# Performance work log

Hardware: AMD Instinct MI355X
Metric: run time of the kernel (lower is better)

Reference implementation:

```python
import jax, jax.numpy as jnp
import numpy as np


def setup_inputs() -> dict:
    key = jax.random.key(0)
    k1, k2 = jax.random.split(key)
    B, S_LOGITS, S_PEN, V = 4, 512, 128, 32000
    logits = jax.random.normal(k1, (B, S_LOGITS, V), dtype=jnp.float32)
    penalty_sequence = jax.random.randint(k2, (B, S_PEN), 0, V, dtype=jnp.int64)
    return {"logits": logits, "penalty_sequence": penalty_sequence, "pad_id": 0}


def reference(logits, penalty_sequence, pad_id):
    B, _, V = logits.shape
    # presence mask over vocab per batch: scatter-max of (id != pad) indicator.
    # Equivalent to onehot(...).sum(-2).clip(max=1) without the (B,S,V) blowup.
    valid = (penalty_sequence != pad_id).astype(logits.dtype)  # (B, S_pen)
    mask = jnp.zeros((B, V), dtype=logits.dtype)
    mask = mask.at[jnp.arange(B)[:, None], penalty_sequence].max(valid)  # (B, V)
    probs = jax.nn.softmax(logits, axis=-1)  # (B, S, V)
    # loss = (mask[:, None, :] * probs).sum(-1)
    return jnp.einsum('bsv,bv->bs', probs, mask)
```

## Files before the change

kernel.cpp:

```cpp
#include <hip/hip_runtime.h>
#include <hip/hip_bf16.h>


#define SPEN 128
#define NWORDS 1000
#define BLOCK 256

__global__ __launch_bounds__(BLOCK) void suppression_loss_kernel(
    const float* __restrict__ logits,
    const int* __restrict__ seq,
    const int* __restrict__ pad_ptr,
    float* __restrict__ out,
    int S, int V) {

    __shared__ unsigned int maskw[NWORDS];
    __shared__ float sd[BLOCK / 64], sn[BLOCK / 64];

    const int row = blockIdx.x;
    const int b   = row / S;
    const int t   = threadIdx.x;
    const int pad = pad_ptr[0];

    for (int i = t; i < NWORDS; i += BLOCK) maskw[i] = 0u;
    __syncthreads();
    if (t < SPEN) {
        int id = seq[b * SPEN + t];
        if (id != pad) atomicOr(&maskw[id >> 5], 1u << (id & 31));
    }
    __syncthreads();

    const float4* lp = (const float4*)(logits + (size_t)row * V);
    const int nvec = V >> 2;
    float d = 0.f, n = 0.f;
    for (int i = t; i < nvec; i += BLOCK) {
        float4 x = lp[i];
        unsigned int nib = (maskw[i >> 3] >> ((i & 7) << 2)) & 0xFu;
        float e0 = __expf(x.x);
        float e1 = __expf(x.y);
        float e2 = __expf(x.z);
        float e3 = __expf(x.w);
        d += (e0 + e1) + (e2 + e3);
        n += (nib & 1u) ? e0 : 0.f;
        n += (nib & 2u) ? e1 : 0.f;
        n += (nib & 4u) ? e2 : 0.f;
        n += (nib & 8u) ? e3 : 0.f;
    }

    #pragma unroll
    for (int off = 32; off > 0; off >>= 1) {
        d += __shfl_down(d, off, 64);
        n += __shfl_down(n, off, 64);
    }
    const int lane = t & 63, wv = t >> 6;
    if (lane == 0) { sd[wv] = d; sn[wv] = n; }
    __syncthreads();
    if (t == 0) {
        float D = (sd[0] + sd[1]) + (sd[2] + sd[3]);
        float N = (sn[0] + sn[1]) + (sn[2] + sn[3]);
        out[row] = N / D;
    }
}

extern "C" void kernel_launch(void* const* d_in, const int* in_sizes, int n_in,
                              void* d_out, int out_size, void* d_ws, size_t ws_size,
                              hipStream_t stream) {
    const float* logits = (const float*)d_in[0];
    const int*   seq    = (const int*)d_in[1];
    const int*   pad    = (const int*)d_in[2];
    float*       out    = (float*)d_out;

    const int B = in_sizes[1] / SPEN;
    const int S = out_size / B;
    const int V = in_sizes[0] / (B * S);
    const int rows = B * S;

    suppression_loss_kernel<<<rows, BLOCK, 0, stream>>>(logits, seq, pad, out, S, V);
}
```

Measured before the change: 357.1 us.

## Precompute deduplicated penalty id list and gather masked logits directly

A small pre-kernel builds a deduplicated list of non-pad penalty ids per batch in workspace. The main kernel then no longer builds a per-block shared bitmask or does per-element mask selects. Instead each thread gathers at most one masked logit and exponentiates it. This removes per-row mask construction, two block barriers, and the select work in the main loop. It adds a second launch and scattered gathers.

```diff
diff --git a/kernel.cpp b/kernel.cpp
--- a/kernel.cpp
+++ b/kernel.cpp
@@ -6,45 +6,71 @@
 #define NWORDS 1000
 #define BLOCK 256
 
+__global__ __launch_bounds__(SPEN) void build_id_list_kernel(
+    const int* __restrict__ seq,
+    const int* __restrict__ pad_ptr,
+    int* __restrict__ cnt_ws,
+    int* __restrict__ ids_ws) {
+
+    __shared__ unsigned int maskw[NWORDS];
+    __shared__ int cnt;
+
+    const int b = blockIdx.x;
+    const int t = threadIdx.x;
+    const int pad = pad_ptr[0];
+
+    for (int i = t; i < NWORDS; i += SPEN) maskw[i] = 0u;
+    if (t == 0) cnt = 0;
+    __syncthreads();
+
+    int id = seq[b * SPEN + t];
+    if (id != pad) {
+        unsigned int bit = 1u << (id & 31);
+        unsigned int old = atomicOr(&maskw[id >> 5], bit);
+        if (!(old & bit)) {
+            int pos = atomicAdd(&cnt, 1);
+            ids_ws[b * SPEN + pos] = id;
+        }
+    }
+    __syncthreads();
+    if (t == 0) cnt_ws[b] = cnt;
+}
+
 __global__ __launch_bounds__(BLOCK) void suppression_loss_kernel(
     const float* __restrict__ logits,
-    const int* __restrict__ seq,
-    const int* __restrict__ pad_ptr,
+    const int* __restrict__ cnt_ws,
+    const int* __restrict__ ids_ws,
     float* __restrict__ out,
     int S, int V) {
 
-    __shared__ unsigned int maskw[NWORDS];
     __shared__ float sd[BLOCK / 64], sn[BLOCK / 64];
 
     const int row = blockIdx.x;
     const int b   = row / S;
     const int t   = threadIdx.x;
-    const int pad = pad_ptr[0];
 
-    for (int i = t; i < NWORDS; i += BLOCK) maskw[i] = 0u;
-    __syncthreads();
-    if (t < SPEN) {
-        int id = seq[b * SPEN + t];
-        if (id != pad) atomicOr(&maskw[id >> 5], 1u << (id & 31));
+    const int cnt = cnt_ws[b];
+    const float* rowp = logits + (size_t)row * V;
+
+    float xv = -3.0e38f;
+    if (t < cnt) {
+        int id = ids_ws[b * SPEN + t];
+        xv = rowp[id];
     }
-    __syncthreads();
 
-    const float4* lp = (const float4*)(logits + (size_t)row * V);
+    const float4* lp = (const float4*)rowp;
     const int nvec = V >> 2;
-    float d = 0.f, n = 0.f;
+    float d = 0.f;
     for (int i = t; i < nvec; i += BLOCK) {
         float4 x = lp[i];
-        unsigned int nib = (maskw[i >> 3] >> ((i & 7) << 2)) & 0xFu;
         float e0 = __expf(x.x);
         float e1 = __expf(x.y);
         float e2 = __expf(x.z);
         float e3 = __expf(x.w);
         d += (e0 + e1) + (e2 + e3);
-        n += (nib & 1u) ? e0 : 0.f;
-        n += (nib & 2u) ? e1 : 0.f;
-        n += (nib & 4u) ? e2 : 0.f;
-        n += (nib & 8u) ? e3 : 0.f;
     }
+
+    float n = __expf(xv);
 
     #pragma unroll
     for (int off = 32; off > 0; off >>= 1) {
@@ -74,5 +100,9 @@
     const int V = in_sizes[0] / (B * S);
     const int rows = B * S;
 
-    suppression_loss_kernel<<<rows, BLOCK, 0, stream>>>(logits, seq, pad, out, S, V);
+    int* cnt_ws = (int*)d_ws;
+    int* ids_ws = cnt_ws + B;
+
+    build_id_list_kernel<<<B, SPEN, 0, stream>>>(seq, pad, cnt_ws, ids_ws);
+    suppression_loss_kernel<<<rows, BLOCK, 0, stream>>>(logits, cnt_ws, ids_ws, out, S, V);
 }
```

Result: no change. 361.2 us (+1.1%).
